# Performance work log

Measured on AMD Instinct MI355X. Metric: run time of the kernel, lower is better.

The kernel has to match this reference:

```python
import jax, jax.numpy as jnp
import numpy as np

B, T, D, U = 32, 1024, 2048, 1024

def setup_inputs() -> dict:
    key = jax.random.key(0)
    ks = jax.random.split(key, 8)
    s_d = 1.0 / np.sqrt(D)
    s_u = 1.0 / np.sqrt(U)
    return {
        "query": jax.random.normal(ks[0], (B, D), dtype=jnp.float32),
        "values": jax.random.normal(ks[1], (B, T, D), dtype=jnp.float32),
        "W1": jax.random.normal(ks[2], (D, U), dtype=jnp.float32) * s_d,
        "b1": jnp.zeros((U,), dtype=jnp.float32),
        "W2": jax.random.normal(ks[3], (D, U), dtype=jnp.float32) * s_d,
        "b2": jnp.zeros((U,), dtype=jnp.float32),
        "V": jax.random.normal(ks[4], (U, 1), dtype=jnp.float32) * s_u,
        "bv": jnp.zeros((1,), dtype=jnp.float32),
    }

def reference(query, values, W1, b1, W2, b2, V, bv):
    # keys: (B, T, U); query proj broadcast over time axis
    keys_proj = jnp.einsum('btd,du->btu', values, W1) + b1
    query_proj = (query @ W2 + b2)[:, None, :]          # (B, 1, U)
    score = jnp.tanh(keys_proj + query_proj) @ V + bv   # (B, T, 1)
    attention_weights = jax.nn.softmax(score, axis=1)   # (B, T, 1)
    context_vector = jnp.sum(attention_weights * values, axis=1)  # (B, D)
    return (context_vector, attention_weights)
```

## Files before the change

kernel.cpp:

```cpp
#include <hip/hip_runtime.h>
#include <math.h>

#define BB 32
#define TS 1024
#define DD 2048
#define UU 1024

typedef _Float16 f16x8 __attribute__((ext_vector_type(8)));
typedef _Float16 f16x2 __attribute__((ext_vector_type(2)));
typedef __fp16 fp16x2 __attribute__((ext_vector_type(2)));
typedef float f32x4 __attribute__((ext_vector_type(4)));

union H8 { f16x8 v; f16x2 p[4]; };

static __device__ inline f16x2 pk(float a, float b) {
  fp16x2 r = __builtin_amdgcn_cvt_pkrtz(a, b);
  return __builtin_bit_cast(f16x2, r);
}

static __device__ inline float fast_tanh(float x) {
  float e = __builtin_amdgcn_exp2f(x * 2.885390081777927f);
  return 1.f - 2.f * __builtin_amdgcn_rcpf(1.f + e);
}

static __device__ inline void gld16(const _Float16* g, _Float16* l) {
  __builtin_amdgcn_global_load_lds(
      (const __attribute__((address_space(1))) void*)g,
      (__attribute__((address_space(3))) void*)l, 16, 0, 0);
}

__global__ void zero_kernel(float* __restrict__ p) {
  p[blockIdx.x * 1024 + threadIdx.x] = 0.f;
}

__global__ __launch_bounds__(256) void qproj_kernel(
    const float* __restrict__ query, const float* __restrict__ W2,
    const float* __restrict__ b1, const float* __restrict__ b2,
    float* __restrict__ qpb) {
  __shared__ float qs[32][128];
  const int u0 = (blockIdx.x & 7) * 128;
  const int dsl = blockIdx.x >> 3;
  const int d0 = dsl * 128;
  const int tid = threadIdx.x;
  const int ul = tid & 127, half = tid >> 7;

  for (int i = tid; i < 32 * 32; i += 256) {
    int b = i >> 5, dq = i & 31;
    *(float4*)&qs[b][dq * 4] = *(const float4*)(query + b * DD + d0 + dq * 4);
  }
  __syncthreads();

  float acc[32];
#pragma unroll
  for (int b = 0; b < 32; ++b) acc[b] = 0.f;

  const float* wcol = W2 + (size_t)(d0 + half * 64) * UU + u0 + ul;
  for (int dd = 0; dd < 64; dd += 4) {
    float w0 = wcol[(size_t)(dd + 0) * UU];
    float w1 = wcol[(size_t)(dd + 1) * UU];
    float w2 = wcol[(size_t)(dd + 2) * UU];
    float w3 = wcol[(size_t)(dd + 3) * UU];
#pragma unroll
    for (int b = 0; b < 32; ++b) {
      float4 q4 = *(const float4*)&qs[b][half * 64 + dd];
      acc[b] += q4.x * w0 + q4.y * w1 + q4.z * w2 + q4.w * w3;
    }
  }

  const int u = u0 + ul;
  const float bias = (dsl == 0 && half == 0) ? (b1[u] + b2[u]) : 0.f;
#pragma unroll
  for (int b = 0; b < 32; ++b) atomicAdd(&qpb[b * UU + u], acc[b] + bias);
}

__global__ __launch_bounds__(256) void pack_values_kernel(
    const float* __restrict__ v, _Float16* __restrict__ vhp) {
  __shared__ _Float16 img[8192];
  const int mTile = blockIdx.x >> 5;
  const int kc = blockIdx.x & 31;
  const int tid = threadIdx.x;

#pragma unroll
  for (int i = 0; i < 4; ++i) {
    int idx = i * 256 + tid;
    int row = idx >> 3, khi = idx & 7;
    const float* src = v + ((size_t)(mTile * 128 + row)) * DD + kc * 64 + khi * 8;
    float4 x = *(const float4*)src;
    float4 y = *(const float4*)(src + 4);
    H8 h;
    h.p[0] = pk(x.x, x.y); h.p[1] = pk(x.z, x.w);
    h.p[2] = pk(y.x, y.y); h.p[3] = pk(y.z, y.w);
    *(f16x8*)&img[(khi * 128 + (row ^ khi)) * 8] = h.v;
  }
  __syncthreads();

  _Float16* out = vhp + ((size_t)mTile * 32 + kc) * 8192;
#pragma unroll
  for (int i = 0; i < 4; ++i) {
    int p = i * 256 + tid;
    int khi = p >> 7, row = p & 127;
    *(f16x8*)(out + (size_t)p * 8) = *(const f16x8*)&img[(khi * 128 + (row ^ khi)) * 8];
  }
}

__global__ __launch_bounds__(256) void pack_w1_kernel(
    const float* __restrict__ W1, _Float16* __restrict__ w1p) {
  __shared__ _Float16 img[8192];
  const int nTile = blockIdx.x >> 5;
  const int kc = blockIdx.x & 31;
  const int tid = threadIdx.x;

#pragma unroll
  for (int i = 0; i < 32; ++i) {
    int idx = i * 256 + tid;
    int ul = idx & 127, kl = idx >> 7;
    float x = W1[(size_t)(kc * 64 + kl) * UU + nTile * 128 + ul];
    int khi = kl >> 3, klo = kl & 7;
    img[(khi * 128 + (ul ^ khi)) * 8 + klo] = (_Float16)x;
  }
  __syncthreads();

  _Float16* out = w1p + ((size_t)nTile * 32 + kc) * 8192;
#pragma unroll
  for (int i = 0; i < 4; ++i) {
    int p = i * 256 + tid;
    int khi = p >> 7, row = p & 127;
    *(f16x8*)(out + (size_t)p * 8) = *(const f16x8*)&img[(khi * 128 + (row ^ khi)) * 8];
  }
}

__global__ __launch_bounds__(512, 2) void score_gemm_p2_kernel(
    const _Float16* __restrict__ vhp, const _Float16* __restrict__ w1p,
    const float* __restrict__ qpb, const float* __restrict__ V,
    float* __restrict__ score) {
  __shared__ _Float16 aS[2][16384];
  __shared__ _Float16 bS[2][16384];

  const int tid = threadIdx.x;
  const int lane = tid & 63, wave = tid >> 6;

  const int swz = (blockIdx.x & 7) * 64 + (blockIdx.x >> 3);
  const int mb = swz >> 2;
  const int nb = swz & 3;

  const int wr = wave >> 2;
  const int wc = wave & 3;
  const int quad = lane >> 4, c16 = lane & 15;

  const _Float16* gA0 = vhp + ((size_t)(2 * mb + 0) * 32) * 8192 + lane * 8;
  const _Float16* gA1 = vhp + ((size_t)(2 * mb + 1) * 32) * 8192 + lane * 8;
  const _Float16* gB0 = w1p + ((size_t)(2 * nb + 0) * 32) * 8192 + lane * 8;
  const _Float16* gB1 = w1p + ((size_t)(2 * nb + 1) * 32) * 8192 + lane * 8;

  f32x4 acc[8][4];
#pragma unroll
  for (int mi = 0; mi < 8; ++mi)
#pragma unroll
    for (int ni = 0; ni < 4; ++ni) acc[mi][ni] = (f32x4)0.f;

  auto STAGE = [&](int kt, int sl) {
#pragma unroll
    for (int j = 0; j < 2; ++j) {
      int s = wave * 2 + j;
      gld16(gA0 + (size_t)kt * 8192 + s * 512, &aS[sl][0 * 8192 + s * 512]);
      gld16(gA1 + (size_t)kt * 8192 + s * 512, &aS[sl][1 * 8192 + s * 512]);
      gld16(gB0 + (size_t)kt * 8192 + s * 512, &bS[sl][0 * 8192 + s * 512]);
      gld16(gB1 + (size_t)kt * 8192 + s * 512, &bS[sl][1 * 8192 + s * 512]);
    }
  };

  STAGE(0, 0);

  const int b = mb >> 2;
  const int nBase = nb * 256;
  float qv[4], vv[4];
#pragma unroll
  for (int ni = 0; ni < 4; ++ni) {
    int ug = nBase + wc * 64 + ni * 16 + c16;
    qv[ni] = qpb[b * UU + ug];
    vv[ni] = V[ug];
  }

  __syncthreads();

  const int aBase = wr * 8192 + c16 * 8;
  const int bBase = (wc >> 1) * 8192 + ((wc & 1) * 64 + c16) * 8;

  for (int it = 0; it < 32; ++it) {
    const int cur = it & 1;

    f16x8 bf[2][4];
#pragma unroll
    for (int hk = 0; hk < 2; ++hk)
#pragma unroll
      for (int ni = 0; ni < 4; ++ni)
        bf[hk][ni] =
            *(const f16x8*)&bS[cur][bBase + (((hk * 4 + quad) * 128) + ni * 16) * 8];

    if (it + 1 < 32) STAGE(it + 1, cur ^ 1);

    __builtin_amdgcn_s_setprio(1);
#pragma unroll
    for (int hk = 0; hk < 2; ++hk) {
#pragma unroll
      for (int mp = 0; mp < 4; ++mp) {
        f16x8 a0 = *(const f16x8*)&aS[cur][aBase +
            (((hk * 4 + quad) * 128) + (mp * 2 + 0) * 16) * 8];
        f16x8 a1 = *(const f16x8*)&aS[cur][aBase +
            (((hk * 4 + quad) * 128) + (mp * 2 + 1) * 16) * 8];
#pragma unroll
        for (int ni = 0; ni < 4; ++ni) {
          acc[mp * 2 + 0][ni] = __builtin_amdgcn_mfma_f32_16x16x32_f16(
              a0, bf[hk][ni], acc[mp * 2 + 0][ni], 0, 0, 0);
          acc[mp * 2 + 1][ni] = __builtin_amdgcn_mfma_f32_16x16x32_f16(
              a1, bf[hk][ni], acc[mp * 2 + 1][ni], 0, 0, 0);
        }
      }
    }
    __builtin_amdgcn_s_setprio(0);

    __syncthreads();
  }

#pragma unroll
  for (int mi = 0; mi < 8; ++mi) {
#pragma unroll
    for (int reg = 0; reg < 4; ++reg) {
      float p = fast_tanh(acc[mi][0][reg] + qv[0]) * vv[0] +
                fast_tanh(acc[mi][1][reg] + qv[1]) * vv[1] +
                fast_tanh(acc[mi][2][reg] + qv[2]) * vv[2] +
                fast_tanh(acc[mi][3][reg] + qv[3]) * vv[3];
      p += __shfl_xor(p, 1, 64);
      p += __shfl_xor(p, 2, 64);
      p += __shfl_xor(p, 4, 64);
      p += __shfl_xor(p, 8, 64);
      if (c16 == 0) {
        int mrow = mb * 256 + wr * 128 + mi * 16 + quad * 4 + reg;
        atomicAdd(&score[mrow], p);
      }
    }
  }
}

__global__ __launch_bounds__(256) void score_gemm_kernel(
    const float* __restrict__ values, const float* __restrict__ W1,
    const float* __restrict__ qpb, const float* __restrict__ V,
    float* __restrict__ score) {
  __shared__ _Float16 aS[4 * 128 * 8];
  __shared__ _Float16 bS[4 * 128 * 8];

  const int tid = threadIdx.x;
  const int mBase = (blockIdx.x >> 3) * 128;
  const int nBase = (blockIdx.x & 7) * 128;

  const int am = tid >> 1;
  const int akh = (tid & 1) * 16;
  const float* aG = values + (size_t)(mBase + am) * DD + akh;
  const int aOff0 = (((tid & 1) * 2) * 128 + am) * 8;
  const int bu2 = (tid & 63) * 2;
  const int bkq = tid >> 6;
  const float* bG = W1 + (size_t)(bkq * 8) * UU + nBase + bu2;
  const int bOff0 = (bkq * 128 + bu2) * 8;

  const int lane = tid & 63;
  const int wave = tid >> 6;
  const int wm = (wave & 1) * 64;
  const int wn = (wave >> 1) * 64;
  const int quad = lane >> 4;
  const int c16 = lane & 15;

  f32x4 acc[4][4];
#pragma unroll
  for (int mi = 0; mi < 4; ++mi)
#pragma unroll
    for (int ni = 0; ni < 4; ++ni) acc[mi][ni] = (f32x4)0.f;

  for (int k0 = 0; k0 < DD; k0 += 32) {
    float4 a0 = *(const float4*)(aG + k0 + 0);
    float4 a1 = *(const float4*)(aG + k0 + 4);
    float4 a2 = *(const float4*)(aG + k0 + 8);
    float4 a3 = *(const float4*)(aG + k0 + 12);
    const float* bRow = bG + (size_t)k0 * UU;
    float2 g0 = *(const float2*)(bRow + 0 * UU);
    float2 g1 = *(const float2*)(bRow + 1 * UU);
    float2 g2 = *(const float2*)(bRow + 2 * UU);
    float2 g3 = *(const float2*)(bRow + 3 * UU);
    float2 g4 = *(const float2*)(bRow + 4 * UU);
    float2 g5 = *(const float2*)(bRow + 5 * UU);
    float2 g6 = *(const float2*)(bRow + 6 * UU);
    float2 g7 = *(const float2*)(bRow + 7 * UU);

    __syncthreads();

    H8 ha0, ha1, hb0, hb1;
    ha0.p[0] = pk(a0.x, a0.y); ha0.p[1] = pk(a0.z, a0.w);
    ha0.p[2] = pk(a1.x, a1.y); ha0.p[3] = pk(a1.z, a1.w);
    ha1.p[0] = pk(a2.x, a2.y); ha1.p[1] = pk(a2.z, a2.w);
    ha1.p[2] = pk(a3.x, a3.y); ha1.p[3] = pk(a3.z, a3.w);
    *(f16x8*)&aS[aOff0] = ha0.v;
    *(f16x8*)&aS[aOff0 + 1024] = ha1.v;

    hb0.p[0] = pk(g0.x, g1.x); hb0.p[1] = pk(g2.x, g3.x);
    hb0.p[2] = pk(g4.x, g5.x); hb0.p[3] = pk(g6.x, g7.x);
    hb1.p[0] = pk(g0.y, g1.y); hb1.p[1] = pk(g2.y, g3.y);
    hb1.p[2] = pk(g4.y, g5.y); hb1.p[3] = pk(g6.y, g7.y);
    *(f16x8*)&bS[bOff0] = hb0.v;
    *(f16x8*)&bS[bOff0 + 8] = hb1.v;

    __syncthreads();

    f16x8 af[4], bf[4];
#pragma unroll
    for (int i = 0; i < 4; ++i) {
      af[i] = *(const f16x8*)&aS[(quad * 128 + wm + i * 16 + c16) * 8];
      bf[i] = *(const f16x8*)&bS[(quad * 128 + wn + i * 16 + c16) * 8];
    }
#pragma unroll
    for (int mi = 0; mi < 4; ++mi)
#pragma unroll
      for (int ni = 0; ni < 4; ++ni)
        acc[mi][ni] = __builtin_amdgcn_mfma_f32_16x16x32_f16(
            af[mi], bf[ni], acc[mi][ni], 0, 0, 0);
  }

  const int b = mBase >> 10;
  float qv[4], vv[4];
#pragma unroll
  for (int ni = 0; ni < 4; ++ni) {
    int ug = nBase + wn + ni * 16 + c16;
    qv[ni] = qpb[b * UU + ug];
    vv[ni] = V[ug];
  }
#pragma unroll
  for (int mi = 0; mi < 4; ++mi) {
#pragma unroll
    for (int reg = 0; reg < 4; ++reg) {
      float p = fast_tanh(acc[mi][0][reg] + qv[0]) * vv[0] +
                fast_tanh(acc[mi][1][reg] + qv[1]) * vv[1] +
                fast_tanh(acc[mi][2][reg] + qv[2]) * vv[2] +
                fast_tanh(acc[mi][3][reg] + qv[3]) * vv[3];
      p += __shfl_xor(p, 1, 64);
      p += __shfl_xor(p, 2, 64);
      p += __shfl_xor(p, 4, 64);
      p += __shfl_xor(p, 8, 64);
      if (c16 == 0) {
        int mrow = mBase + wm + mi * 16 + quad * 4 + reg;
        atomicAdd(&score[mrow], p);
      }
    }
  }
}

__global__ __launch_bounds__(1024) void softmax_kernel(float* __restrict__ sw) {
  __shared__ float red[16];
  const int b = blockIdx.x;
  const int tid = threadIdx.x;
  const int wid = tid >> 6, lane = tid & 63;
  float* s = sw + b * TS;

  const float v = s[tid];

  float m = v;
#pragma unroll
  for (int off = 32; off > 0; off >>= 1) m = fmaxf(m, __shfl_xor(m, off, 64));
  if (lane == 0) red[wid] = m;
  __syncthreads();
  float mm = red[0];
#pragma unroll
  for (int i = 1; i < 16; ++i) mm = fmaxf(mm, red[i]);
  __syncthreads();

  const float e = expf(v - mm);
  float sum = e;
#pragma unroll
  for (int off = 32; off > 0; off >>= 1) sum += __shfl_xor(sum, off, 64);
  if (lane == 0) red[wid] = sum;
  __syncthreads();
  float tot = 0.f;
#pragma unroll
  for (int i = 0; i < 16; ++i) tot += red[i];

  s[tid] = e * (1.f / tot);
}

__global__ __launch_bounds__(256) void context_p_kernel(
    const _Float16* __restrict__ vhp, const float* __restrict__ weights,
    float* __restrict__ context) {
  __shared__ float wl[TS];
  const int b = blockIdx.x >> 5;
  const int kc = blockIdx.x & 31;
  const int tid = threadIdx.x;
  const int lane = tid & 63, wave = tid >> 6;

  for (int i = tid; i < TS; i += 256) wl[i] = weights[b * TS + i];
  __syncthreads();

  const int khiA = wave;
  const int khiB = wave + 4;

  float acc0[8], acc1[8];
#pragma unroll
  for (int j = 0; j < 8; ++j) { acc0[j] = 0.f; acc1[j] = 0.f; }

  for (int mt8 = 0; mt8 < 8; ++mt8) {
    const _Float16* base = vhp + ((size_t)(b * 8 + mt8) * 32 + kc) * 8192;
    const float* wrow = &wl[mt8 * 128];
#pragma unroll
    for (int half = 0; half < 2; ++half) {
      const int row = half * 64 + lane;
      const float wt = wrow[row];
      f16x8 vA = *(const f16x8*)&base[(khiA * 128 + row) * 8];
      f16x8 vB = *(const f16x8*)&base[(khiB * 128 + row) * 8];
#pragma unroll
      for (int j = 0; j < 8; ++j) {
        acc0[j] += wt * (float)vA[j];
        acc1[j] += wt * (float)vB[j];
      }
    }
  }

#pragma unroll
  for (int j = 0; j < 8; ++j) {
    float a = acc0[j], c = acc1[j];
#pragma unroll
    for (int off = 1; off < 64; off <<= 1) {
      a += __shfl_xor(a, off, 64);
      c += __shfl_xor(c, off, 64);
    }
    acc0[j] = a; acc1[j] = c;
  }

  if (lane == 0) {
    float* dst = context + b * DD + kc * 64;
#pragma unroll
    for (int j = 0; j < 8; ++j) {
      dst[khiA * 8 + j] = acc0[j];
      dst[khiB * 8 + j] = acc1[j];
    }
  }
}

__global__ __launch_bounds__(1024) void context_kernel(
    const float* __restrict__ values, const float* __restrict__ weights,
    float* __restrict__ context) {
  __shared__ float wl[TS];
  __shared__ float4 part[15][64];
  const int b = blockIdx.x >> 3;
  const int d0 = (blockIdx.x & 7) * 256;
  const int tid = threadIdx.x;
  const int slice = tid >> 6, dl = tid & 63;

  wl[tid] = weights[b * TS + tid];
  __syncthreads();

  const float* vb = values + ((size_t)b * TS + slice * 64) * DD + d0 + dl * 4;
  float4 acc = {0.f, 0.f, 0.f, 0.f};
#pragma unroll 8
  for (int t = 0; t < 64; ++t) {
    float w = wl[slice * 64 + t];
    float4 v4 = *(const float4*)(vb + (size_t)t * DD);
    acc.x += w * v4.x; acc.y += w * v4.y;
    acc.z += w * v4.z; acc.w += w * v4.w;
  }

  if (slice) part[slice - 1][dl] = acc;
  __syncthreads();
  if (slice == 0) {
#pragma unroll
    for (int i = 0; i < 15; ++i) {
      float4 p = part[i][dl];
      acc.x += p.x; acc.y += p.y; acc.z += p.z; acc.w += p.w;
    }
    *(float4*)(context + b * DD + d0 + dl * 4) = acc;
  }
}

extern "C" void kernel_launch(void* const* d_in, const int* in_sizes, int n_in,
                              void* d_out, int out_size, void* d_ws, size_t ws_size,
                              hipStream_t stream) {
  const float* query  = (const float*)d_in[0];
  const float* values = (const float*)d_in[1];
  const float* W1     = (const float*)d_in[2];
  const float* b1     = (const float*)d_in[3];
  const float* W2     = (const float*)d_in[4];
  const float* b2     = (const float*)d_in[5];
  const float* V      = (const float*)d_in[6];

  float* out = (float*)d_out;
  float* context = out;
  float* weights = out + BB * DD;

  float* qpb   = context;
  float* score = weights;

  const size_t need = (size_t)BB * TS * DD * 2 + (size_t)DD * UU * 2;
  const bool big_ws = ws_size >= need;

  zero_kernel<<<96, 1024, 0, stream>>>(out);
  qproj_kernel<<<128, 256, 0, stream>>>(query, W2, b1, b2, qpb);

  if (big_ws) {
    _Float16* vhp = (_Float16*)d_ws;
    _Float16* w1p = vhp + (size_t)BB * TS * DD;
    pack_values_kernel<<<256 * 32, 256, 0, stream>>>(values, vhp);
    pack_w1_kernel<<<8 * 32, 256, 0, stream>>>(W1, w1p);
    score_gemm_p2_kernel<<<(BB * TS / 256) * (UU / 256), 512, 0, stream>>>(
        vhp, w1p, qpb, V, score);
    softmax_kernel<<<BB, 1024, 0, stream>>>(score);
    context_p_kernel<<<BB * 32, 256, 0, stream>>>(vhp, weights, context);
  } else {
    score_gemm_kernel<<<(BB * TS / 128) * (UU / 128), 256, 0, stream>>>(
        values, W1, qpb, V, score);
    softmax_kernel<<<BB, 1024, 0, stream>>>(score);
    context_kernel<<<BB * 8, 1024, 0, stream>>>(values, weights, context);
  }
}
```

Baseline: 594.4 us.

## Split GEMM main loop into four barrier-fenced phases interleaving loads and MFMA

Restructures the score GEMM main loop into four sub-phases per k-tile. Each phase issues a quarter of the next tile's global-to-LDS loads, reads a subset of A/B fragments from LDS, then runs 16 MFMAs, with explicit s_waitcnt and s_barrier fences in place of one __syncthreads per tile. The aim is finer-grained overlap of memory traffic with matrix math and lower register pressure from holding fewer fragments at once. In exchange it adds many more barriers per iteration and relies on hand-tuned vmcnt counts being correct.

```diff
diff --git a/kernel.cpp b/kernel.cpp
--- a/kernel.cpp
+++ b/kernel.cpp
@@ -129,7 +129,7 @@
   }
 }
 
-__global__ __launch_bounds__(512, 2) void score_gemm_p2_kernel(
+__global__ __launch_bounds__(512, 2) void score_gemm_p3_kernel(
     const _Float16* __restrict__ vhp, const _Float16* __restrict__ w1p,
     const float* __restrict__ qpb, const float* __restrict__ V,
     float* __restrict__ score) {
@@ -158,18 +158,18 @@
 #pragma unroll
     for (int ni = 0; ni < 4; ++ni) acc[mi][ni] = (f32x4)0.f;
 
-  auto STAGE = [&](int kt, int sl) {
-#pragma unroll
-    for (int j = 0; j < 2; ++j) {
-      int s = wave * 2 + j;
-      gld16(gA0 + (size_t)kt * 8192 + s * 512, &aS[sl][0 * 8192 + s * 512]);
-      gld16(gA1 + (size_t)kt * 8192 + s * 512, &aS[sl][1 * 8192 + s * 512]);
-      gld16(gB0 + (size_t)kt * 8192 + s * 512, &bS[sl][0 * 8192 + s * 512]);
-      gld16(gB1 + (size_t)kt * 8192 + s * 512, &bS[sl][1 * 8192 + s * 512]);
-    }
+  auto STAGE_A = [&](int kt, int sl, int kh) {
+    gld16(gA0 + (size_t)kt * 8192 + kh * 4096 + wave * 512,
+          &aS[sl][0 * 8192 + kh * 4096 + wave * 512]);
+    gld16(gA1 + (size_t)kt * 8192 + kh * 4096 + wave * 512,
+          &aS[sl][1 * 8192 + kh * 4096 + wave * 512]);
   };
-
-  STAGE(0, 0);
+  auto STAGE_B = [&](int kt, int sl, int kh) {
+    gld16(gB0 + (size_t)kt * 8192 + kh * 4096 + wave * 512,
+          &bS[sl][0 * 8192 + kh * 4096 + wave * 512]);
+    gld16(gB1 + (size_t)kt * 8192 + kh * 4096 + wave * 512,
+          &bS[sl][1 * 8192 + kh * 4096 + wave * 512]);
+  };
 
   const int b = mb >> 2;
   const int nBase = nb * 256;
@@ -181,46 +181,110 @@
     vv[ni] = V[ug];
   }
 
-  __syncthreads();
+  STAGE_A(0, 0, 0); STAGE_B(0, 0, 0); STAGE_A(0, 0, 1); STAGE_B(0, 0, 1);
+  asm volatile("s_waitcnt vmcnt(4)" ::: "memory");
+  __builtin_amdgcn_s_barrier();
+  __builtin_amdgcn_sched_barrier(0);
 
   const int aBase = wr * 8192 + c16 * 8;
   const int bBase = (wc >> 1) * 8192 + ((wc & 1) * 64 + c16) * 8;
 
-  for (int it = 0; it < 32; ++it) {
-    const int cur = it & 1;
-
-    f16x8 bf[2][4];
-#pragma unroll
-    for (int hk = 0; hk < 2; ++hk)
+  f16x8 bf[4];
+  auto DS_B = [&](int sl, int hk) {
+#pragma unroll
+    for (int ni = 0; ni < 4; ++ni)
+      bf[ni] = *(const f16x8*)&bS[sl][bBase + (hk * 4 + quad) * 1024 + ni * 128];
+  };
+  auto DS_A = [&](int sl, int hk, int g, f16x8* af) {
+#pragma unroll
+    for (int mi = 0; mi < 4; ++mi)
+      af[mi] = *(const f16x8*)&aS[sl][aBase + (hk * 4 + quad) * 1024 + (g * 4 + mi) * 128];
+  };
+  auto MFMA16 = [&](int g, f16x8* af) {
+    __builtin_amdgcn_s_setprio(1);
+#pragma unroll
+    for (int mi = 0; mi < 4; ++mi)
 #pragma unroll
       for (int ni = 0; ni < 4; ++ni)
-        bf[hk][ni] =
-            *(const f16x8*)&bS[cur][bBase + (((hk * 4 + quad) * 128) + ni * 16) * 8];
-
-    if (it + 1 < 32) STAGE(it + 1, cur ^ 1);
-
-    __builtin_amdgcn_s_setprio(1);
-#pragma unroll
-    for (int hk = 0; hk < 2; ++hk) {
-#pragma unroll
-      for (int mp = 0; mp < 4; ++mp) {
-        f16x8 a0 = *(const f16x8*)&aS[cur][aBase +
-            (((hk * 4 + quad) * 128) + (mp * 2 + 0) * 16) * 8];
-        f16x8 a1 = *(const f16x8*)&aS[cur][aBase +
-            (((hk * 4 + quad) * 128) + (mp * 2 + 1) * 16) * 8];
-#pragma unroll
-        for (int ni = 0; ni < 4; ++ni) {
-          acc[mp * 2 + 0][ni] = __builtin_amdgcn_mfma_f32_16x16x32_f16(
-              a0, bf[hk][ni], acc[mp * 2 + 0][ni], 0, 0, 0);
-          acc[mp * 2 + 1][ni] = __builtin_amdgcn_mfma_f32_16x16x32_f16(
-              a1, bf[hk][ni], acc[mp * 2 + 1][ni], 0, 0, 0);
-        }
-      }
-    }
+        acc[g * 4 + mi][ni] = __builtin_amdgcn_mfma_f32_16x16x32_f16(
+            af[mi], bf[ni], acc[g * 4 + mi][ni], 0, 0, 0);
     __builtin_amdgcn_s_setprio(0);
-
-    __syncthreads();
-  }
+  };
+#define LGKM0_FENCE                                    \
+  asm volatile("s_waitcnt lgkmcnt(0)" ::: "memory");   \
+  __builtin_amdgcn_sched_barrier(0)
+
+  for (int t = 0; t < 31; ++t) {
+    const int sl = t & 1, so = sl ^ 1;
+    {
+      f16x8 af[4];
+      DS_B(sl, 0); DS_A(sl, 0, 0, af);
+      STAGE_A(t + 1, so, 0);
+      __builtin_amdgcn_s_barrier();
+      LGKM0_FENCE;
+      MFMA16(0, af);
+      __builtin_amdgcn_s_barrier();
+    }
+    {
+      f16x8 af[4];
+      DS_A(sl, 0, 1, af);
+      STAGE_B(t + 1, so, 0);
+      __builtin_amdgcn_s_barrier();
+      LGKM0_FENCE;
+      MFMA16(1, af);
+      asm volatile("s_waitcnt vmcnt(4)" ::: "memory");
+      __builtin_amdgcn_s_barrier();
+      __builtin_amdgcn_sched_barrier(0);
+    }
+    {
+      f16x8 af[4];
+      DS_B(sl, 1); DS_A(sl, 1, 0, af);
+      STAGE_A(t + 1, so, 1);
+      __builtin_amdgcn_s_barrier();
+      LGKM0_FENCE;
+      MFMA16(0, af);
+      __builtin_amdgcn_s_barrier();
+    }
+    {
+      f16x8 af[4];
+      DS_A(sl, 1, 1, af);
+      STAGE_B(t + 1, so, 1);
+      __builtin_amdgcn_s_barrier();
+      LGKM0_FENCE;
+      MFMA16(1, af);
+      asm volatile("s_waitcnt vmcnt(4)" ::: "memory");
+      __builtin_amdgcn_s_barrier();
+      __builtin_amdgcn_sched_barrier(0);
+    }
+  }
+  {
+    f16x8 af[4];
+    DS_B(1, 0); DS_A(1, 0, 0, af);
+    __builtin_amdgcn_s_barrier();
+    LGKM0_FENCE;
+    MFMA16(0, af);
+    __builtin_amdgcn_s_barrier();
+
+    DS_A(1, 0, 1, af);
+    __builtin_amdgcn_s_barrier();
+    LGKM0_FENCE;
+    MFMA16(1, af);
+    asm volatile("s_waitcnt vmcnt(0)" ::: "memory");
+    __builtin_amdgcn_s_barrier();
+    __builtin_amdgcn_sched_barrier(0);
+
+    DS_B(1, 1); DS_A(1, 1, 0, af);
+    __builtin_amdgcn_s_barrier();
+    LGKM0_FENCE;
+    MFMA16(0, af);
+    __builtin_amdgcn_s_barrier();
+
+    DS_A(1, 1, 1, af);
+    __builtin_amdgcn_s_barrier();
+    LGKM0_FENCE;
+    MFMA16(1, af);
+  }
+#undef LGKM0_FENCE
 
 #pragma unroll
   for (int mi = 0; mi < 8; ++mi) {
@@ -504,7 +568,7 @@
     _Float16* w1p = vhp + (size_t)BB * TS * DD;
     pack_values_kernel<<<256 * 32, 256, 0, stream>>>(values, vhp);
     pack_w1_kernel<<<8 * 32, 256, 0, stream>>>(W1, w1p);
-    score_gemm_p2_kernel<<<(BB * TS / 256) * (UU / 256), 512, 0, stream>>>(
+    score_gemm_p3_kernel<<<(BB * TS / 256) * (UU / 256), 512, 0, stream>>>(
         vhp, w1p, qpb, V, score);
     softmax_kernel<<<BB, 1024, 0, stream>>>(score);
     context_p_kernel<<<BB * 32, 256, 0, stream>>>(vhp, weights, context);
```

Result: no change. 594.5 us (+0.0%).

## Deepen score GEMM pipeline to four smaller LDS stages with explicit vmcnt waits

Applied to the files above, without the earlier changes.

The score GEMM's shared-memory pipeline changes from two 64-wide K stages to four 32-wide K stages, with three loads in flight. Plain __syncthreads are replaced by explicit s_waitcnt vmcnt plus s_barrier, so each wave waits only for the oldest outstanding stage. The goal is to hide global-load latency behind MFMA work. The cost is twice as many iterations and barriers, and correctness now depends on the hand-counted vmcnt values.

```diff
diff --git a/kernel.cpp b/kernel.cpp
--- a/kernel.cpp
+++ b/kernel.cpp
@@ -129,12 +129,12 @@
   }
 }
 
-__global__ __launch_bounds__(512, 2) void score_gemm_p2_kernel(
+__global__ __launch_bounds__(512, 2) void score_gemm_p5_kernel(
     const _Float16* __restrict__ vhp, const _Float16* __restrict__ w1p,
     const float* __restrict__ qpb, const float* __restrict__ V,
     float* __restrict__ score) {
-  __shared__ _Float16 aS[2][16384];
-  __shared__ _Float16 bS[2][16384];
+  __shared__ _Float16 aS[4][8192];
+  __shared__ _Float16 bS[4][8192];
 
   const int tid = threadIdx.x;
   const int lane = tid & 63, wave = tid >> 6;
@@ -159,17 +159,11 @@
     for (int ni = 0; ni < 4; ++ni) acc[mi][ni] = (f32x4)0.f;
 
   auto STAGE = [&](int kt, int sl) {
-#pragma unroll
-    for (int j = 0; j < 2; ++j) {
-      int s = wave * 2 + j;
-      gld16(gA0 + (size_t)kt * 8192 + s * 512, &aS[sl][0 * 8192 + s * 512]);
-      gld16(gA1 + (size_t)kt * 8192 + s * 512, &aS[sl][1 * 8192 + s * 512]);
-      gld16(gB0 + (size_t)kt * 8192 + s * 512, &bS[sl][0 * 8192 + s * 512]);
-      gld16(gB1 + (size_t)kt * 8192 + s * 512, &bS[sl][1 * 8192 + s * 512]);
-    }
+    gld16(gA0 + (size_t)kt * 4096 + wave * 512, &aS[sl][0 * 4096 + wave * 512]);
+    gld16(gA1 + (size_t)kt * 4096 + wave * 512, &aS[sl][1 * 4096 + wave * 512]);
+    gld16(gB0 + (size_t)kt * 4096 + wave * 512, &bS[sl][0 * 4096 + wave * 512]);
+    gld16(gB1 + (size_t)kt * 4096 + wave * 512, &bS[sl][1 * 4096 + wave * 512]);
   };
-
-  STAGE(0, 0);
 
   const int b = mb >> 2;
   const int nBase = nb * 256;
@@ -181,45 +175,47 @@
     vv[ni] = V[ug];
   }
 
-  __syncthreads();
-
-  const int aBase = wr * 8192 + c16 * 8;
-  const int bBase = (wc >> 1) * 8192 + ((wc & 1) * 64 + c16) * 8;
-
-  for (int it = 0; it < 32; ++it) {
-    const int cur = it & 1;
-
-    f16x8 bf[2][4];
-#pragma unroll
-    for (int hk = 0; hk < 2; ++hk)
-#pragma unroll
-      for (int ni = 0; ni < 4; ++ni)
-        bf[hk][ni] =
-            *(const f16x8*)&bS[cur][bBase + (((hk * 4 + quad) * 128) + ni * 16) * 8];
-
-    if (it + 1 < 32) STAGE(it + 1, cur ^ 1);
+  STAGE(0, 0); STAGE(1, 1); STAGE(2, 2);
+  asm volatile("s_waitcnt vmcnt(8)" ::: "memory");
+  __builtin_amdgcn_s_barrier();
+
+  const int aBase = wr * 4096 + quad * 1024 + c16 * 8;
+  const int bBase = (wc >> 1) * 4096 + quad * 1024 + ((wc & 1) * 64 + c16) * 8;
+
+#pragma unroll 4
+  for (int t = 0; t < 64; ++t) {
+    const int sl = t & 3;
+    if (t < 61) STAGE(t + 3, (t + 3) & 3);
+
+    f16x8 bf[4];
+#pragma unroll
+    for (int ni = 0; ni < 4; ++ni)
+      bf[ni] = *(const f16x8*)&bS[sl][bBase + ni * 128];
 
     __builtin_amdgcn_s_setprio(1);
 #pragma unroll
-    for (int hk = 0; hk < 2; ++hk) {
-#pragma unroll
-      for (int mp = 0; mp < 4; ++mp) {
-        f16x8 a0 = *(const f16x8*)&aS[cur][aBase +
-            (((hk * 4 + quad) * 128) + (mp * 2 + 0) * 16) * 8];
-        f16x8 a1 = *(const f16x8*)&aS[cur][aBase +
-            (((hk * 4 + quad) * 128) + (mp * 2 + 1) * 16) * 8];
-#pragma unroll
-        for (int ni = 0; ni < 4; ++ni) {
-          acc[mp * 2 + 0][ni] = __builtin_amdgcn_mfma_f32_16x16x32_f16(
-              a0, bf[hk][ni], acc[mp * 2 + 0][ni], 0, 0, 0);
-          acc[mp * 2 + 1][ni] = __builtin_amdgcn_mfma_f32_16x16x32_f16(
-              a1, bf[hk][ni], acc[mp * 2 + 1][ni], 0, 0, 0);
-        }
+    for (int g = 0; g < 2; ++g) {
+      f16x8 af[4];
+#pragma unroll
+      for (int mi = 0; mi < 4; ++mi)
+        af[mi] = *(const f16x8*)&aS[sl][aBase + (g * 4 + mi) * 128];
+#pragma unroll
+      for (int mi = 0; mi < 4; ++mi)
+#pragma unroll
+        for (int ni = 0; ni < 4; ++ni)
+          acc[g * 4 + mi][ni] = __builtin_amdgcn_mfma_f32_16x16x32_f16(
+              af[mi], bf[ni], acc[g * 4 + mi][ni], 0, 0, 0);
+    }
+    __builtin_amdgcn_s_setprio(0);
+
+    if (t < 63) {
+      if (t < 61) {
+        asm volatile("s_waitcnt vmcnt(4)" ::: "memory");
+      } else {
+        asm volatile("s_waitcnt vmcnt(0)" ::: "memory");
       }
-    }
-    __builtin_amdgcn_s_setprio(0);
-
-    __syncthreads();
+      __builtin_amdgcn_s_barrier();
+    }
   }
 
 #pragma unroll
@@ -504,7 +500,7 @@
     _Float16* w1p = vhp + (size_t)BB * TS * DD;
     pack_values_kernel<<<256 * 32, 256, 0, stream>>>(values, vhp);
     pack_w1_kernel<<<8 * 32, 256, 0, stream>>>(W1, w1p);
-    score_gemm_p2_kernel<<<(BB * TS / 256) * (UU / 256), 512, 0, stream>>>(
+    score_gemm_p5_kernel<<<(BB * TS / 256) * (UU / 256), 512, 0, stream>>>(
         vhp, w1p, qpb, V, score);
     softmax_kernel<<<BB, 1024, 0, stream>>>(score);
     context_p_kernel<<<BB * 32, 256, 0, stream>>>(vhp, weights, context);
```

After: 574.1 us. -3.4%, faster.
